# Kernel optimization log

Hardware: AMD Instinct MI355X
Metric: run time of the kernel (lower is better)

The kernel has to match this reference:

```python
import jax, jax.numpy as jnp
import numpy as np

EPS = 1e-5

def _mlp(x, W1, b1, W2, b2):
    h = jax.nn.gelu(x @ W1 + b1, approximate=False)
    return h @ W2 + b2

def _ln(x, g, b):
    m = jnp.mean(x, axis=-1, keepdims=True)
    v = jnp.mean((x - m) ** 2, axis=-1, keepdims=True)
    return (x - m) * jax.lax.rsqrt(v + EPS) * g + b

def setup_inputs() -> dict:
    key = jax.random.key(0)
    B, N, D = 4, 256, 128
    ks = jax.random.split(key, 32)
    s = 0.02
    inp = {
        "node_h": jax.random.normal(ks[0], (B, N, D), jnp.float32),
        "pair_h": jax.random.normal(ks[1], (B, N, N, D), jnp.float32),
        "node_mask": jax.random.randint(ks[2], (B, N), 0, 2, jnp.int32),
        "edge_mask": jax.random.randint(ks[3], (B, N, N), 0, 2, jnp.int32),
        # node_from_pair MLP: 3D -> 2D -> D
        "nfp_W1": jax.random.normal(ks[4], (3 * D, 2 * D), jnp.float32) * s,
        "nfp_b1": jnp.zeros((2 * D,), jnp.float32),
        "nfp_W2": jax.random.normal(ks[5], (2 * D, D), jnp.float32) * s,
        "nfp_b2": jnp.zeros((D,), jnp.float32),
        # pair_from_node MLP: 5D -> 2D -> D
        "pfn_W1": jax.random.normal(ks[6], (5 * D, 2 * D), jnp.float32) * s,
        "pfn_b1": jnp.zeros((2 * D,), jnp.float32),
        "pfn_W2": jax.random.normal(ks[7], (2 * D, D), jnp.float32) * s,
        "pfn_b2": jnp.zeros((D,), jnp.float32),
        # node_ff: D -> 4D -> D
        "nff_W1": jax.random.normal(ks[8], (D, 4 * D), jnp.float32) * s,
        "nff_b1": jnp.zeros((4 * D,), jnp.float32),
        "nff_W2": jax.random.normal(ks[9], (4 * D, D), jnp.float32) * s,
        "nff_b2": jnp.zeros((D,), jnp.float32),
        # pair_ff: D -> 4D -> D
        "pff_W1": jax.random.normal(ks[10], (D, 4 * D), jnp.float32) * s,
        "pff_b1": jnp.zeros((4 * D,), jnp.float32),
        "pff_W2": jax.random.normal(ks[11], (4 * D, D), jnp.float32) * s,
        "pff_b2": jnp.zeros((D,), jnp.float32),
        # gates: 2D -> D, sigmoid
        "og_W": jax.random.normal(ks[12], (2 * D, D), jnp.float32) * s,
        "og_b": jnp.zeros((D,), jnp.float32),
        "ig_W": jax.random.normal(ks[13], (2 * D, D), jnp.float32) * s,
        "ig_b": jnp.zeros((D,), jnp.float32),
        # LayerNorms
        "nn1_g": jnp.ones((D,), jnp.float32), "nn1_b": jnp.zeros((D,), jnp.float32),
        "nn2_g": jnp.ones((D,), jnp.float32), "nn2_b": jnp.zeros((D,), jnp.float32),
        "pn1_g": jnp.ones((D,), jnp.float32), "pn1_b": jnp.zeros((D,), jnp.float32),
        "pn2_g": jnp.ones((D,), jnp.float32), "pn2_b": jnp.zeros((D,), jnp.float32),
    }
    return inp

def reference(node_h, pair_h, node_mask, edge_mask,
              nfp_W1, nfp_b1, nfp_W2, nfp_b2,
              pfn_W1, pfn_b1, pfn_W2, pfn_b2,
              nff_W1, nff_b1, nff_W2, nff_b2,
              pff_W1, pff_b1, pff_W2, pff_b2,
              og_W, og_b, ig_W, ig_b,
              nn1_g, nn1_b, nn2_g, nn2_b,
              pn1_g, pn1_b, pn2_g, pn2_b):
    vp = edge_mask.astype(jnp.float32)                       # [B,N,N]
    pair_m = pair_h * vp[..., None]                          # masked pairs
    out_deg = jnp.clip(vp.sum(axis=2), 1.0)[..., None]       # [B,N,1]
    in_deg = jnp.clip(vp.sum(axis=1), 1.0)[..., None]        # [B,N,1]
    out_ctx_raw = pair_m.sum(axis=2) / out_deg               # [B,N,D]
    in_ctx_raw = pair_m.sum(axis=1) / in_deg                 # [B,N,D]
    out_g = jax.nn.sigmoid(jnp.concatenate([node_h, out_ctx_raw], -1) @ og_W + og_b)
    in_g = jax.nn.sigmoid(jnp.concatenate([node_h, in_ctx_raw], -1) @ ig_W + ig_b)
    node_upd = _mlp(jnp.concatenate([node_h, out_g * out_ctx_raw, in_g * in_ctx_raw], -1),
                    nfp_W1, nfp_b1, nfp_W2, nfp_b2)
    node_h = _ln(node_h + node_upd, nn1_g, nn1_b)
    node_h = _ln(node_h + _mlp(node_h, nff_W1, nff_b1, nff_W2, nff_b2), nn2_g, nn2_b)
    node_h = node_h * node_mask.astype(jnp.float32)[..., None]

    B, N, D = node_h.shape
    hi = jnp.broadcast_to(node_h[:, :, None, :], (B, N, N, D))
    hj = jnp.broadcast_to(node_h[:, None, :, :], (B, N, N, D))
    feat = jnp.concatenate([pair_h, hi, hj, hi - hj, hi * hj], -1)  # [B,N,N,5D]
    pair_upd = _mlp(feat, pfn_W1, pfn_b1, pfn_W2, pfn_b2)
    pair_h = _ln(pair_h + pair_upd, pn1_g, pn1_b)
    pair_h = _ln(pair_h + _mlp(pair_h, pff_W1, pff_b1, pff_W2, pff_b2), pn2_g, pn2_b)
    pair_h = pair_h * vp[..., None]
    return (node_h, pair_h)
```

## Files before the change

kernel.cpp:

```cpp
#include <hip/hip_runtime.h>
#include <hip/hip_bf16.h>

#define DI __device__ __forceinline__

typedef float f32x4 __attribute__((ext_vector_type(4)));
typedef float f32x2 __attribute__((ext_vector_type(2)));
typedef short s16x8 __attribute__((ext_vector_type(8)));
typedef short s16x4 __attribute__((ext_vector_type(4)));

DI short f2bf(float x) {
  union { float f; unsigned u; } v; v.f = x;
  unsigned r = v.u + 0x7fffu + ((v.u >> 16) & 1u);
  return (short)(r >> 16);
}

DI float bf2f(short x) {
  union { unsigned u; float f; } v;
  v.u = ((unsigned)(unsigned short)x) << 16;
  return v.f;
}

DI float gelu_f(float x) {
  return 0.5f * x * (1.0f + erff(x * 0.70710678118654752f));
}

DI f32x4 mfma16(s16x8 a, s16x8 b, f32x4 c) {
  return __builtin_amdgcn_mfma_f32_16x16x32_bf16(a, b, c, 0, 0, 0);
}

__global__ __launch_bounds__(256) void prep_kernel(
    const float* __restrict__ pfnW1, const float* __restrict__ pfnW2,
    const float* __restrict__ pffW1, const float* __restrict__ pffW2,
    short* __restrict__ W1b, float* __restrict__ Wu, short* __restrict__ W2T,
    short* __restrict__ W1Tp, short* __restrict__ W2Tp) {
  int idx = blockIdx.x * 256 + threadIdx.x;
  if (idx < 98304) {
    int n = idx / 384, k = idx % 384;
    float v;
    if (k < 128) v = pfnW1[k * 256 + n];
    else if (k < 256) v = pfnW1[(128 + k) * 256 + n] - pfnW1[(256 + k) * 256 + n];
    else v = pfnW1[(256 + k) * 256 + n];
    W1b[idx] = f2bf(v);
    return;
  }
  idx -= 98304;
  if (idx < 32768) {
    int k = idx / 256, n = idx % 256;
    Wu[idx] = pfnW1[(128 + k) * 256 + n] + pfnW1[(384 + k) * 256 + n];
    return;
  }
  idx -= 32768;
  if (idx < 32768) {
    int n = idx / 256, k = idx % 256;
    W2T[idx] = f2bf(pfnW2[k * 128 + n]);
    return;
  }
  idx -= 32768;
  if (idx < 65536) {
    int n = idx / 128, k = idx % 128;
    W1Tp[idx] = f2bf(pffW1[k * 512 + n]);
    return;
  }
  idx -= 65536;
  if (idx < 65536) {
    int n = idx / 512, k = idx % 512;
    W2Tp[idx] = f2bf(pffW2[k * 128 + n]);
  }
}

__global__ __launch_bounds__(256) void ctx_kernel(
    const float* __restrict__ pair_h, const int* __restrict__ edge_mask,
    float* __restrict__ out_ctx, float* __restrict__ in_ctx) {
  __shared__ float sacc[2][128];
  __shared__ float sdeg[2];
  const int wg = blockIdx.x;
  const int t = threadIdx.x;
  const int half = t >> 7, d = t & 127;
  const bool outmode = wg < 1024;
  const int w2 = outmode ? wg : wg - 1024;
  const int b = w2 >> 8, x = w2 & 255;

  float acc = 0.f, deg = 0.f;
  for (int y0 = 0; y0 < 256; y0 += 2) {
    const int y = y0 + half;
    int row;
    if (outmode) row = (b * 256 + x) * 256 + y;
    else row = (b * 256 + y) * 256 + x;
    const int m = edge_mask[row];
    if (m) {
      acc += pair_h[(long)row * 128 + d];
      deg += 1.f;
    }
  }
  sacc[half][d] = acc;
  if (d == 0) sdeg[half] = deg;
  __syncthreads();
  if (t < 128) {
    float tot = sacc[0][d] + sacc[1][d];
    float dg = fmaxf(sdeg[0] + sdeg[1], 1.f);
    float* dst = outmode ? out_ctx : in_ctx;
    dst[(b * 256 + x) * 128 + d] = tot / dg;
  }
}

__global__ __launch_bounds__(256) void node_kernel(
    const float* __restrict__ node_h, const float* __restrict__ out_ctx,
    const float* __restrict__ in_ctx, const int* __restrict__ node_mask,
    const float* __restrict__ ogW, const float* __restrict__ ogb,
    const float* __restrict__ igW, const float* __restrict__ igb,
    const float* __restrict__ nW1, const float* __restrict__ nb1,
    const float* __restrict__ nW2, const float* __restrict__ nb2,
    const float* __restrict__ fW1, const float* __restrict__ fb1,
    const float* __restrict__ fW2, const float* __restrict__ fb2,
    const float* __restrict__ g1, const float* __restrict__ be1,
    const float* __restrict__ g2, const float* __restrict__ be2,
    float* __restrict__ out_node, short* __restrict__ node_bf) {
  __shared__ float sh[4][1792];
  const int t = threadIdx.x;
  const int wv = t >> 6, lane = t & 63;
  float* const xn = sh[wv];
  float* const xo = sh[wv] + 256;
  float* const xi = sh[wv] + 512;
  float* const hh = sh[wv] + 768;
  const int row0 = blockIdx.x * 8 + wv * 2;

#pragma unroll
  for (int r = 0; r < 2; ++r) {
    const int row = row0 + r;
#pragma unroll
    for (int c = 0; c < 2; ++c) {
      const int col = lane + 64 * c;
      xn[r * 128 + col] = node_h[row * 128 + col];
      xo[r * 128 + col] = out_ctx[row * 128 + col];
      xi[r * 128 + col] = in_ctx[row * 128 + col];
    }
  }
  __syncthreads();

  {
    float ao[2][2], ai[2][2];
#pragma unroll
    for (int c = 0; c < 2; ++c) {
      const int col = lane + 64 * c;
      ao[0][c] = ao[1][c] = ogb[col];
      ai[0][c] = ai[1][c] = igb[col];
    }
    for (int k = 0; k < 256; ++k) {
      float xo0, xo1, xi0, xi1;
      if (k < 128) {
        xo0 = xi0 = xn[k];
        xo1 = xi1 = xn[128 + k];
      } else {
        xo0 = xo[k - 128]; xo1 = xo[k];
        xi0 = xi[k - 128]; xi1 = xi[k];
      }
#pragma unroll
      for (int c = 0; c < 2; ++c) {
        const int col = lane + 64 * c;
        const float wo = ogW[k * 128 + col], wi = igW[k * 128 + col];
        ao[0][c] += xo0 * wo; ao[1][c] += xo1 * wo;
        ai[0][c] += xi0 * wi; ai[1][c] += xi1 * wi;
      }
    }
#pragma unroll
    for (int c = 0; c < 2; ++c) {
      const int col = lane + 64 * c;
#pragma unroll
      for (int r = 0; r < 2; ++r) {
        const float go = 1.f / (1.f + __expf(-ao[r][c]));
        const float gi = 1.f / (1.f + __expf(-ai[r][c]));
        xo[r * 128 + col] *= go;
        xi[r * 128 + col] *= gi;
      }
    }
  }
  __syncthreads();

  {
    float a1[2][4];
#pragma unroll
    for (int c = 0; c < 4; ++c) {
      const int col = lane + 64 * c;
      a1[0][c] = a1[1][c] = nb1[col];
    }
    for (int k = 0; k < 384; ++k) {
      const float* src = (k < 128) ? xn : (k < 256) ? xo : xi;
      const int kk = k & 127;
      const float x0 = src[kk], x1 = src[128 + kk];
#pragma unroll
      for (int c = 0; c < 4; ++c) {
        const int col = lane + 64 * c;
        const float w = nW1[k * 256 + col];
        a1[0][c] += x0 * w; a1[1][c] += x1 * w;
      }
    }
#pragma unroll
    for (int c = 0; c < 4; ++c) {
      const int col = lane + 64 * c;
      hh[col] = gelu_f(a1[0][c]);
      hh[512 + col] = gelu_f(a1[1][c]);
    }
  }
  __syncthreads();
  {
    float a2[2][2];
#pragma unroll
    for (int c = 0; c < 2; ++c) {
      const int col = lane + 64 * c;
      a2[0][c] = a2[1][c] = nb2[col];
    }
    for (int k = 0; k < 256; ++k) {
      const float h0 = hh[k], h1 = hh[512 + k];
#pragma unroll
      for (int c = 0; c < 2; ++c) {
        const int col = lane + 64 * c;
        const float w = nW2[k * 128 + col];
        a2[0][c] += h0 * w; a2[1][c] += h1 * w;
      }
    }
#pragma unroll
    for (int r = 0; r < 2; ++r) {
      float v0 = xn[r * 128 + lane] + a2[r][0];
      float v1 = xn[r * 128 + lane + 64] + a2[r][1];
      float s = v0 + v1, ss = v0 * v0 + v1 * v1;
#pragma unroll
      for (int off = 1; off < 64; off <<= 1) {
        s += __shfl_xor(s, off, 64);
        ss += __shfl_xor(ss, off, 64);
      }
      const float m = s * (1.f / 128.f);
      const float var = ss * (1.f / 128.f) - m * m;
      const float rs = rsqrtf(var + 1e-5f);
      xn[r * 128 + lane] = (v0 - m) * rs * g1[lane] + be1[lane];
      xn[r * 128 + lane + 64] = (v1 - m) * rs * g1[lane + 64] + be1[lane + 64];
    }
  }
  __syncthreads();

  {
    float af[2][8];
#pragma unroll
    for (int c = 0; c < 8; ++c) {
      const int col = lane + 64 * c;
      af[0][c] = af[1][c] = fb1[col];
    }
    for (int k = 0; k < 128; ++k) {
      const float x0 = xn[k], x1 = xn[128 + k];
#pragma unroll
      for (int c = 0; c < 8; ++c) {
        const int col = lane + 64 * c;
        const float w = fW1[k * 512 + col];
        af[0][c] += x0 * w; af[1][c] += x1 * w;
      }
    }
#pragma unroll
    for (int c = 0; c < 8; ++c) {
      const int col = lane + 64 * c;
      hh[col] = gelu_f(af[0][c]);
      hh[512 + col] = gelu_f(af[1][c]);
    }
  }
  __syncthreads();
  {
    float a2[2][2];
#pragma unroll
    for (int c = 0; c < 2; ++c) {
      const int col = lane + 64 * c;
      a2[0][c] = a2[1][c] = fb2[col];
    }
    for (int k = 0; k < 512; ++k) {
      const float h0 = hh[k], h1 = hh[512 + k];
#pragma unroll
      for (int c = 0; c < 2; ++c) {
        const int col = lane + 64 * c;
        const float w = fW2[k * 128 + col];
        a2[0][c] += h0 * w; a2[1][c] += h1 * w;
      }
    }
#pragma unroll
    for (int r = 0; r < 2; ++r) {
      const int row = row0 + r;
      float v0 = xn[r * 128 + lane] + a2[r][0];
      float v1 = xn[r * 128 + lane + 64] + a2[r][1];
      float s = v0 + v1, ss = v0 * v0 + v1 * v1;
#pragma unroll
      for (int off = 1; off < 64; off <<= 1) {
        s += __shfl_xor(s, off, 64);
        ss += __shfl_xor(ss, off, 64);
      }
      const float m = s * (1.f / 128.f);
      const float var = ss * (1.f / 128.f) - m * m;
      const float rs = rsqrtf(var + 1e-5f);
      const float msk = (float)node_mask[row];
      const float o0 = ((v0 - m) * rs * g2[lane] + be2[lane]) * msk;
      const float o1 = ((v1 - m) * rs * g2[lane + 64] + be2[lane + 64]) * msk;
      out_node[row * 128 + lane] = o0;
      out_node[row * 128 + lane + 64] = o1;
      node_bf[row * 128 + lane] = f2bf(o0);
      node_bf[row * 128 + lane + 64] = f2bf(o1);
    }
  }
}

__global__ __launch_bounds__(256) void u_kernel(
    const float* __restrict__ out_node, const float* __restrict__ Wu,
    const float* __restrict__ b1, float* __restrict__ u_all) {
  __shared__ float nrow[8][128];
  const int t = threadIdx.x;
  const int r0 = blockIdx.x * 8;
  {
    const int r = t >> 5, c = (t & 31) * 4;
    *(f32x4*)&nrow[r][c] = *(const f32x4*)(out_node + (r0 + r) * 128 + c);
  }
  __syncthreads();
  float acc[8];
  const float bb = b1[t];
#pragma unroll
  for (int r = 0; r < 8; ++r) acc[r] = bb;
  for (int k = 0; k < 128; ++k) {
    const float w = Wu[k * 256 + t];
#pragma unroll
    for (int r = 0; r < 8; ++r) acc[r] += nrow[r][k] * w;
  }
#pragma unroll
  for (int r = 0; r < 8; ++r) u_all[(r0 + r) * 256 + t] = acc[r];
}

__global__ __launch_bounds__(512, 4) void pair_kernel(
    const float* __restrict__ pair_h, const short* __restrict__ node_bf,
    const int* __restrict__ edge_mask, const short* __restrict__ W1b,
    const short* __restrict__ W2T, const short* __restrict__ W1Tp,
    const short* __restrict__ W2Tp, const float* __restrict__ u_all,
    const float* __restrict__ b2, const float* __restrict__ b1p,
    const float* __restrict__ b2p, const float* __restrict__ g1,
    const float* __restrict__ be1, const float* __restrict__ g2,
    const float* __restrict__ be2, float* __restrict__ out_pair) {
  constexpr int OFF_A = 0, OFF_H1 = 0, OFF_Y = 0, OFF_H2 = 16384,
                OFF_SCR = 49152;
  __shared__ __align__(16) char smem[81920];

  const int t = threadIdx.x;
  const int wg = blockIdx.x;
  const int b = wg >> 10, rem = wg & 1023;
  const int i = rem >> 2, j0 = (rem & 3) << 6;
  const int bi = (b << 8) + i;
  const long rowbase = (long)bi * 256 + j0;

  const int lane = t & 63, wv = t >> 6;
  const int lr = lane & 15, lq = lane >> 4;
  const int swz = (lr & 7) << 4;

  {
    const int r = t >> 3, oc = t & 7, c0 = oc * 16;
    const int rsw = (r & 7) << 4;
    const float* prow = pair_h + (rowbase + r) * 128 + c0;
    const short* hjrow = node_bf + (b * 256 + j0 + r) * 128 + c0;
    const short* hirow = node_bf + (b * 256 + i) * 128 + c0;
    char* arow = smem + OFF_A + r * 768;
    s16x8 pr[2], hj[2], hi[2];
#pragma unroll
    for (int h = 0; h < 2; ++h) {
      f32x4 p0 = *(const f32x4*)(prow + h * 8);
      f32x4 p1 = *(const f32x4*)(prow + h * 8 + 4);
      s16x8 sp;
#pragma unroll
      for (int e = 0; e < 4; ++e) { sp[e] = f2bf(p0[e]); sp[e + 4] = f2bf(p1[e]); }
      pr[h] = sp;
      hj[h] = *(const s16x8*)(hjrow + h * 8);
      hi[h] = *(const s16x8*)(hirow + h * 8);
    }
#pragma unroll
    for (int h = 0; h < 2; ++h) {
      *(s16x8*)(arow + ((c0 * 2 + h * 16) ^ rsw)) = pr[h];
      *(s16x8*)(arow + ((256 + c0 * 2 + h * 16) ^ rsw)) = hj[h];
      s16x8 pd;
#pragma unroll
      for (int e = 0; e < 8; ++e) pd[e] = f2bf(bf2f(hi[h][e]) * bf2f(hj[h][e]));
      *(s16x8*)(arow + ((512 + c0 * 2 + h * 16) ^ rsw)) = pd;
    }
  }
  __syncthreads();

  f32x4 acc1[4][2];
#pragma unroll
  for (int jt = 0; jt < 4; ++jt)
#pragma unroll
    for (int nt = 0; nt < 2; ++nt) acc1[jt][nt] = {0.f, 0.f, 0.f, 0.f};
  {
    const int nb = wv * 32;
    const short* wp0 = W1b + (nb + lr) * 384 + lq * 8;
    const short* wp1 = W1b + (nb + 16 + lr) * 384 + lq * 8;
    s16x8 w0 = *(const s16x8*)wp0;
    s16x8 w1 = *(const s16x8*)wp1;
#pragma unroll
    for (int ks = 0; ks < 12; ++ks) {
      s16x8 nw0 = w0, nw1 = w1;
      if (ks < 11) {
        nw0 = *(const s16x8*)(wp0 + (ks + 1) * 32);
        nw1 = *(const s16x8*)(wp1 + (ks + 1) * 32);
      }
      s16x8 d[4];
#pragma unroll
      for (int jt = 0; jt < 4; ++jt)
        d[jt] = *(const s16x8*)(smem + OFF_A +
                                (((jt * 16 + lr) * 768 + ks * 64 + lq * 16) ^ swz));
#pragma unroll
      for (int jt = 0; jt < 4; ++jt) {
        acc1[jt][0] = mfma16(w0, d[jt], acc1[jt][0]);
        acc1[jt][1] = mfma16(w1, d[jt], acc1[jt][1]);
      }
      w0 = nw0; w1 = nw1;
    }
  }
  __syncthreads();
  {
    const int nb = wv * 32;
#pragma unroll
    for (int nt = 0; nt < 2; ++nt) {
      const int n0 = nb + nt * 16 + lq * 4;
      f32x4 bu = *(const f32x4*)(u_all + bi * 256 + n0);
#pragma unroll
      for (int jt = 0; jt < 4; ++jt) {
        const int j = jt * 16 + lr;
        s16x4 hp;
#pragma unroll
        for (int v = 0; v < 4; ++v) hp[v] = f2bf(gelu_f(acc1[jt][nt][v] + bu[v]));
        *(s16x4*)(smem + OFF_H1 + ((j * 512 + n0 * 2) ^ swz)) = hp;
      }
    }
  }
  __syncthreads();

  const int jb = (wv >> 2) * 32, nb2 = (wv & 3) * 32;
  f32x4 x1v[2][2];
  {
    f32x4 acc2[2][2];
#pragma unroll
    for (int jt = 0; jt < 2; ++jt)
#pragma unroll
      for (int nt = 0; nt < 2; ++nt) acc2[jt][nt] = {0.f, 0.f, 0.f, 0.f};
    const short* wp0 = W2T + (nb2 + lr) * 256 + lq * 8;
    const short* wp1 = W2T + (nb2 + 16 + lr) * 256 + lq * 8;
    s16x8 w0 = *(const s16x8*)wp0;
    s16x8 w1 = *(const s16x8*)wp1;
#pragma unroll
    for (int ks = 0; ks < 8; ++ks) {
      s16x8 nw0 = w0, nw1 = w1;
      if (ks < 7) {
        nw0 = *(const s16x8*)(wp0 + (ks + 1) * 32);
        nw1 = *(const s16x8*)(wp1 + (ks + 1) * 32);
      }
      s16x8 d[2];
#pragma unroll
      for (int jt = 0; jt < 2; ++jt)
        d[jt] = *(const s16x8*)(smem + OFF_H1 +
                                (((jb + jt * 16 + lr) * 512 + ks * 64 + lq * 16) ^ swz));
#pragma unroll
      for (int jt = 0; jt < 2; ++jt) {
        acc2[jt][0] = mfma16(w0, d[jt], acc2[jt][0]);
        acc2[jt][1] = mfma16(w1, d[jt], acc2[jt][1]);
      }
      w0 = nw0; w1 = nw1;
    }
#pragma unroll
    for (int nt = 0; nt < 2; ++nt) {
      const int n0 = nb2 + nt * 16 + lq * 4;
      f32x4 bv = *(const f32x4*)(b2 + n0);
#pragma unroll
      for (int jt = 0; jt < 2; ++jt) {
        const int j = jb + jt * 16 + lr;
        f32x4 pr = *(const f32x4*)(pair_h + (rowbase + j) * 128 + n0);
        x1v[jt][nt] = acc2[jt][nt] + bv + pr;
      }
    }
  }
  {
    float s[2], ss[2];
#pragma unroll
    for (int jt = 0; jt < 2; ++jt) {
      s[jt] = 0.f; ss[jt] = 0.f;
#pragma unroll
      for (int nt = 0; nt < 2; ++nt)
#pragma unroll
        for (int v = 0; v < 4; ++v) {
          const float x = x1v[jt][nt][v];
          s[jt] += x; ss[jt] += x * x;
        }
      s[jt] += __shfl_xor(s[jt], 16, 64);
      ss[jt] += __shfl_xor(ss[jt], 16, 64);
      s[jt] += __shfl_xor(s[jt], 32, 64);
      ss[jt] += __shfl_xor(ss[jt], 32, 64);
    }
    if (lq == 0) {
#pragma unroll
      for (int jt = 0; jt < 2; ++jt) {
        const int j = jb + jt * 16 + lr;
        f32x2 p = {s[jt], ss[jt]};
        *(f32x2*)(smem + OFF_SCR + j * 32 + (wv & 3) * 8) = p;
      }
    }
    __syncthreads();
    float lnm[2], lnr[2];
#pragma unroll
    for (int jt = 0; jt < 2; ++jt) {
      const int j = jb + jt * 16 + lr;
      f32x4 pA = *(const f32x4*)(smem + OFF_SCR + j * 32);
      f32x4 pB = *(const f32x4*)(smem + OFF_SCR + j * 32 + 16);
      const float S = pA[0] + pA[2] + pB[0] + pB[2];
      const float SS = pA[1] + pA[3] + pB[1] + pB[3];
      const float m = S * (1.f / 128.f);
      const float var = SS * (1.f / 128.f) - m * m;
      lnm[jt] = m;
      lnr[jt] = rsqrtf(var + 1e-5f);
    }
#pragma unroll
    for (int nt = 0; nt < 2; ++nt) {
      const int n0 = nb2 + nt * 16 + lq * 4;
      f32x4 gv = *(const f32x4*)(g1 + n0);
      f32x4 bv = *(const f32x4*)(be1 + n0);
#pragma unroll
      for (int jt = 0; jt < 2; ++jt) {
        const int j = jb + jt * 16 + lr;
        s16x4 yp;
#pragma unroll
        for (int v = 0; v < 4; ++v)
          yp[v] = f2bf((x1v[jt][nt][v] - lnm[jt]) * lnr[jt] * gv[v] + bv[v]);
        *(s16x4*)(smem + OFF_Y + ((j * 256 + n0 * 2) ^ swz)) = yp;
      }
    }
  }
  __syncthreads();

#pragma unroll
  for (int p = 0; p < 2; ++p) {
    f32x4 acc3[4][2];
#pragma unroll
    for (int jt = 0; jt < 4; ++jt)
#pragma unroll
      for (int nt = 0; nt < 2; ++nt) acc3[jt][nt] = {0.f, 0.f, 0.f, 0.f};
    const int nb3 = wv * 64 + p * 32;
    const short* wp0 = W1Tp + (nb3 + lr) * 128 + lq * 8;
    const short* wp1 = W1Tp + (nb3 + 16 + lr) * 128 + lq * 8;
    s16x8 w0 = *(const s16x8*)wp0;
    s16x8 w1 = *(const s16x8*)wp1;
#pragma unroll
    for (int ks = 0; ks < 4; ++ks) {
      s16x8 nw0 = w0, nw1 = w1;
      if (ks < 3) {
        nw0 = *(const s16x8*)(wp0 + (ks + 1) * 32);
        nw1 = *(const s16x8*)(wp1 + (ks + 1) * 32);
      }
      s16x8 d[4];
#pragma unroll
      for (int jt = 0; jt < 4; ++jt)
        d[jt] = *(const s16x8*)(smem + OFF_Y +
                                (((jt * 16 + lr) * 256 + ks * 64 + lq * 16) ^ swz));
#pragma unroll
      for (int jt = 0; jt < 4; ++jt) {
        acc3[jt][0] = mfma16(w0, d[jt], acc3[jt][0]);
        acc3[jt][1] = mfma16(w1, d[jt], acc3[jt][1]);
      }
      w0 = nw0; w1 = nw1;
    }
#pragma unroll
    for (int nt = 0; nt < 2; ++nt) {
      const int n0 = nb3 + nt * 16 + lq * 4;
      f32x4 bv = *(const f32x4*)(b1p + n0);
#pragma unroll
      for (int jt = 0; jt < 4; ++jt) {
        const int j = jt * 16 + lr;
        s16x4 hp;
#pragma unroll
        for (int v = 0; v < 4; ++v) hp[v] = f2bf(gelu_f(acc3[jt][nt][v] + bv[v]));
        *(s16x4*)(smem + OFF_H2 + ((j * 1024 + n0 * 2) ^ swz)) = hp;
      }
    }
  }
  __syncthreads();

  f32x4 x2v[2][2];
  {
    f32x4 acc4[2][2];
#pragma unroll
    for (int jt = 0; jt < 2; ++jt)
#pragma unroll
      for (int nt = 0; nt < 2; ++nt) acc4[jt][nt] = {0.f, 0.f, 0.f, 0.f};
    const short* wp0 = W2Tp + (nb2 + lr) * 512 + lq * 8;
    const short* wp1 = W2Tp + (nb2 + 16 + lr) * 512 + lq * 8;
    s16x8 w0 = *(const s16x8*)wp0;
    s16x8 w1 = *(const s16x8*)wp1;
#pragma unroll
    for (int ks = 0; ks < 16; ++ks) {
      s16x8 nw0 = w0, nw1 = w1;
      if (ks < 15) {
        nw0 = *(const s16x8*)(wp0 + (ks + 1) * 32);
        nw1 = *(const s16x8*)(wp1 + (ks + 1) * 32);
      }
      s16x8 d[2];
#pragma unroll
      for (int jt = 0; jt < 2; ++jt)
        d[jt] = *(const s16x8*)(smem + OFF_H2 +
                                (((jb + jt * 16 + lr) * 1024 + ks * 64 + lq * 16) ^ swz));
#pragma unroll
      for (int jt = 0; jt < 2; ++jt) {
        acc4[jt][0] = mfma16(w0, d[jt], acc4[jt][0]);
        acc4[jt][1] = mfma16(w1, d[jt], acc4[jt][1]);
      }
      w0 = nw0; w1 = nw1;
    }
#pragma unroll
    for (int nt = 0; nt < 2; ++nt) {
      const int n0 = nb2 + nt * 16 + lq * 4;
      f32x4 bv = *(const f32x4*)(b2p + n0);
#pragma unroll
      for (int jt = 0; jt < 2; ++jt) {
        const int j = jb + jt * 16 + lr;
        s16x4 yv = *(const s16x4*)(smem + OFF_Y + ((j * 256 + n0 * 2) ^ swz));
        f32x4 yr;
#pragma unroll
        for (int v = 0; v < 4; ++v) yr[v] = bf2f(yv[v]);
        x2v[jt][nt] = acc4[jt][nt] + bv + yr;
      }
    }
  }
  {
    float s[2], ss[2];
#pragma unroll
    for (int jt = 0; jt < 2; ++jt) {
      s[jt] = 0.f; ss[jt] = 0.f;
#pragma unroll
      for (int nt = 0; nt < 2; ++nt)
#pragma unroll
        for (int v = 0; v < 4; ++v) {
          const float x = x2v[jt][nt][v];
          s[jt] += x; ss[jt] += x * x;
        }
      s[jt] += __shfl_xor(s[jt], 16, 64);
      ss[jt] += __shfl_xor(ss[jt], 16, 64);
      s[jt] += __shfl_xor(s[jt], 32, 64);
      ss[jt] += __shfl_xor(ss[jt], 32, 64);
    }
    __syncthreads();
    if (lq == 0) {
#pragma unroll
      for (int jt = 0; jt < 2; ++jt) {
        const int j = jb + jt * 16 + lr;
        f32x2 p = {s[jt], ss[jt]};
        *(f32x2*)(smem + OFF_SCR + j * 32 + (wv & 3) * 8) = p;
      }
    }
    __syncthreads();
    float lnm[2], lnr[2], vp[2];
#pragma unroll
    for (int jt = 0; jt < 2; ++jt) {
      const int j = jb + jt * 16 + lr;
      f32x4 pA = *(const f32x4*)(smem + OFF_SCR + j * 32);
      f32x4 pB = *(const f32x4*)(smem + OFF_SCR + j * 32 + 16);
      const float S = pA[0] + pA[2] + pB[0] + pB[2];
      const float SS = pA[1] + pA[3] + pB[1] + pB[3];
      const float m = S * (1.f / 128.f);
      const float var = SS * (1.f / 128.f) - m * m;
      lnm[jt] = m;
      lnr[jt] = rsqrtf(var + 1e-5f);
      vp[jt] = (float)edge_mask[(long)bi * 256 + j0 + j];
    }
#pragma unroll
    for (int nt = 0; nt < 2; ++nt) {
      const int n0 = nb2 + nt * 16 + lq * 4;
      f32x4 gv = *(const f32x4*)(g2 + n0);
      f32x4 bv = *(const f32x4*)(be2 + n0);
#pragma unroll
      for (int jt = 0; jt < 2; ++jt) {
        const int j = jb + jt * 16 + lr;
        f32x4 o;
#pragma unroll
        for (int v = 0; v < 4; ++v)
          o[v] = ((x2v[jt][nt][v] - lnm[jt]) * lnr[jt] * gv[v] + bv[v]) * vp[jt];
        *(f32x4*)(out_pair + (rowbase + j) * 128 + n0) = o;
      }
    }
  }
}

extern "C" void kernel_launch(void* const* d_in, const int* in_sizes, int n_in,
                              void* d_out, int out_size, void* d_ws,
                              size_t ws_size, hipStream_t stream) {
  const float* node_h = (const float*)d_in[0];
  const float* pair_h = (const float*)d_in[1];
  const int* node_mask = (const int*)d_in[2];
  const int* edge_mask = (const int*)d_in[3];
  const float* nfp_W1 = (const float*)d_in[4];
  const float* nfp_b1 = (const float*)d_in[5];
  const float* nfp_W2 = (const float*)d_in[6];
  const float* nfp_b2 = (const float*)d_in[7];
  const float* pfn_W1 = (const float*)d_in[8];
  const float* pfn_b1 = (const float*)d_in[9];
  const float* pfn_W2 = (const float*)d_in[10];
  const float* pfn_b2 = (const float*)d_in[11];
  const float* nff_W1 = (const float*)d_in[12];
  const float* nff_b1 = (const float*)d_in[13];
  const float* nff_W2 = (const float*)d_in[14];
  const float* nff_b2 = (const float*)d_in[15];
  const float* pff_W1 = (const float*)d_in[16];
  const float* pff_b1 = (const float*)d_in[17];
  const float* pff_W2 = (const float*)d_in[18];
  const float* pff_b2 = (const float*)d_in[19];
  const float* og_W = (const float*)d_in[20];
  const float* og_b = (const float*)d_in[21];
  const float* ig_W = (const float*)d_in[22];
  const float* ig_b = (const float*)d_in[23];
  const float* nn1_g = (const float*)d_in[24];
  const float* nn1_b = (const float*)d_in[25];
  const float* nn2_g = (const float*)d_in[26];
  const float* nn2_b = (const float*)d_in[27];
  const float* pn1_g = (const float*)d_in[28];
  const float* pn1_b = (const float*)d_in[29];
  const float* pn2_g = (const float*)d_in[30];
  const float* pn2_b = (const float*)d_in[31];

  char* ws = (char*)d_ws;
  short* W1b = (short*)(ws);
  short* W2T = (short*)(ws + 196608);
  short* W1Tp = (short*)(ws + 262144);
  short* W2Tp = (short*)(ws + 393216);
  float* Wu = (float*)(ws + 524288);
  float* out_ctx = (float*)(ws + 655360);
  float* in_ctx = (float*)(ws + 1179648);
  short* node_bf = (short*)(ws + 1703936);
  float* u_all = (float*)(ws + 1966080);

  float* out_node = (float*)d_out;
  float* out_pair = (float*)d_out + 131072;

  prep_kernel<<<1152, 256, 0, stream>>>(pfn_W1, pfn_W2, pff_W1, pff_W2, W1b,
                                        Wu, W2T, W1Tp, W2Tp);
  ctx_kernel<<<2048, 256, 0, stream>>>(pair_h, edge_mask, out_ctx, in_ctx);
  node_kernel<<<128, 256, 0, stream>>>(
      node_h, out_ctx, in_ctx, node_mask, og_W, og_b, ig_W, ig_b, nfp_W1,
      nfp_b1, nfp_W2, nfp_b2, nff_W1, nff_b1, nff_W2, nff_b2, nn1_g, nn1_b,
      nn2_g, nn2_b, out_node, node_bf);
  u_kernel<<<128, 256, 0, stream>>>(out_node, Wu, pfn_b1, u_all);
  pair_kernel<<<4096, 512, 0, stream>>>(
      pair_h, node_bf, edge_mask, W1b, W2T, W1Tp, W2Tp, u_all, pfn_b2, pff_b1,
      pff_b2, pn1_g, pn1_b, pn2_g, pn2_b, out_pair);
}
```

Before: 625.4 us.

## Split pair FF into two K-halves, shrink LDS, fuse small kernels, fast GELU

```diff
diff --git a/kernel.cpp b/kernel.cpp
--- a/kernel.cpp
+++ b/kernel.cpp
@@ -7,6 +7,8 @@
 typedef float f32x2 __attribute__((ext_vector_type(2)));
 typedef short s16x8 __attribute__((ext_vector_type(8)));
 typedef short s16x4 __attribute__((ext_vector_type(4)));
+typedef unsigned u32x2 __attribute__((ext_vector_type(2)));
+typedef unsigned u32x4 __attribute__((ext_vector_type(4)));
 
 DI short f2bf(float x) {
   union { float f; unsigned u; } v; v.f = x;
@@ -20,66 +22,75 @@
   return v.f;
 }
 
+DI unsigned cvt_pk(float lo, float hi) {
+  unsigned r;
+  asm("v_cvt_pk_bf16_f32 %0, %1, %2" : "=v"(r) : "v"(lo), "v"(hi));
+  return r;
+}
+
+DI s16x8 pack8(f32x4 a, f32x4 b) {
+  union { u32x4 u; s16x8 s; } r;
+  r.u[0] = cvt_pk(a[0], a[1]); r.u[1] = cvt_pk(a[2], a[3]);
+  r.u[2] = cvt_pk(b[0], b[1]); r.u[3] = cvt_pk(b[2], b[3]);
+  return r.s;
+}
+
 DI float gelu_f(float x) {
-  return 0.5f * x * (1.0f + erff(x * 0.70710678118654752f));
-}
-
-DI f32x4 mfma16(s16x8 a, s16x8 b, f32x4 c) {
-  return __builtin_amdgcn_mfma_f32_16x16x32_bf16(a, b, c, 0, 0, 0);
-}
-
-__global__ __launch_bounds__(256) void prep_kernel(
+  const float e = __expf(-x * fmaf(x * x, 0.0713548162f, 1.5957691216f));
+  return __fdividef(x, 1.f + e);
+}
+
+__global__ __launch_bounds__(256) void prep_ctx_kernel(
+    const float* __restrict__ pair_h, const int* __restrict__ edge_mask,
     const float* __restrict__ pfnW1, const float* __restrict__ pfnW2,
     const float* __restrict__ pffW1, const float* __restrict__ pffW2,
     short* __restrict__ W1b, float* __restrict__ Wu, short* __restrict__ W2T,
-    short* __restrict__ W1Tp, short* __restrict__ W2Tp) {
-  int idx = blockIdx.x * 256 + threadIdx.x;
-  if (idx < 98304) {
-    int n = idx / 384, k = idx % 384;
-    float v;
-    if (k < 128) v = pfnW1[k * 256 + n];
-    else if (k < 256) v = pfnW1[(128 + k) * 256 + n] - pfnW1[(256 + k) * 256 + n];
-    else v = pfnW1[(256 + k) * 256 + n];
-    W1b[idx] = f2bf(v);
-    return;
-  }
-  idx -= 98304;
-  if (idx < 32768) {
-    int k = idx / 256, n = idx % 256;
-    Wu[idx] = pfnW1[(128 + k) * 256 + n] + pfnW1[(384 + k) * 256 + n];
-    return;
-  }
-  idx -= 32768;
-  if (idx < 32768) {
-    int n = idx / 256, k = idx % 256;
-    W2T[idx] = f2bf(pfnW2[k * 128 + n]);
-    return;
-  }
-  idx -= 32768;
-  if (idx < 65536) {
-    int n = idx / 128, k = idx % 128;
-    W1Tp[idx] = f2bf(pffW1[k * 512 + n]);
-    return;
-  }
-  idx -= 65536;
-  if (idx < 65536) {
-    int n = idx / 512, k = idx % 512;
-    W2Tp[idx] = f2bf(pffW2[k * 128 + n]);
-  }
-}
-
-__global__ __launch_bounds__(256) void ctx_kernel(
-    const float* __restrict__ pair_h, const int* __restrict__ edge_mask,
+    short* __restrict__ W1Tp, short* __restrict__ W2Tp,
     float* __restrict__ out_ctx, float* __restrict__ in_ctx) {
   __shared__ float sacc[2][128];
   __shared__ float sdeg[2];
+  const int t = threadIdx.x;
+  if (blockIdx.x >= 2048) {
+    int idx = (blockIdx.x - 2048) * 256 + t;
+    if (idx < 98304) {
+      int n = idx / 384, k = idx % 384;
+      float v;
+      if (k < 128) v = pfnW1[k * 256 + n];
+      else if (k < 256) v = pfnW1[(128 + k) * 256 + n] - pfnW1[(256 + k) * 256 + n];
+      else v = pfnW1[(256 + k) * 256 + n];
+      W1b[idx] = f2bf(v);
+      return;
+    }
+    idx -= 98304;
+    if (idx < 32768) {
+      int k = idx / 256, n = idx % 256;
+      Wu[idx] = pfnW1[(128 + k) * 256 + n] + pfnW1[(384 + k) * 256 + n];
+      return;
+    }
+    idx -= 32768;
+    if (idx < 32768) {
+      int n = idx / 256, k = idx % 256;
+      W2T[idx] = f2bf(pfnW2[k * 128 + n]);
+      return;
+    }
+    idx -= 32768;
+    if (idx < 65536) {
+      int n = idx / 128, k = idx % 128;
+      W1Tp[idx] = f2bf(pffW1[k * 512 + n]);
+      return;
+    }
+    idx -= 65536;
+    if (idx < 65536) {
+      int n = idx / 512, k = idx % 512;
+      W2Tp[idx] = f2bf(pffW2[k * 128 + n]);
+    }
+    return;
+  }
   const int wg = blockIdx.x;
-  const int t = threadIdx.x;
   const int half = t >> 7, d = t & 127;
   const bool outmode = wg < 1024;
   const int w2 = outmode ? wg : wg - 1024;
   const int b = w2 >> 8, x = w2 & 255;
-
   float acc = 0.f, deg = 0.f;
   for (int y0 = 0; y0 < 256; y0 += 2) {
     const int y = y0 + half;
@@ -114,8 +125,11 @@
     const float* __restrict__ fW2, const float* __restrict__ fb2,
     const float* __restrict__ g1, const float* __restrict__ be1,
     const float* __restrict__ g2, const float* __restrict__ be2,
-    float* __restrict__ out_node, short* __restrict__ node_bf) {
+    const float* __restrict__ Wu, const float* __restrict__ ub1,
+    float* __restrict__ out_node, short* __restrict__ node_bf,
+    float* __restrict__ u_all) {
   __shared__ float sh[4][1792];
+  __shared__ float fin[8][128];
   const int t = threadIdx.x;
   const int wv = t >> 6, lane = t & 63;
   float* const xn = sh[wv];
@@ -298,35 +312,29 @@
       out_node[row * 128 + lane + 64] = o1;
       node_bf[row * 128 + lane] = f2bf(o0);
       node_bf[row * 128 + lane + 64] = f2bf(o1);
-    }
-  }
-}
-
-__global__ __launch_bounds__(256) void u_kernel(
-    const float* __restrict__ out_node, const float* __restrict__ Wu,
-    const float* __restrict__ b1, float* __restrict__ u_all) {
-  __shared__ float nrow[8][128];
-  const int t = threadIdx.x;
-  const int r0 = blockIdx.x * 8;
-  {
-    const int r = t >> 5, c = (t & 31) * 4;
-    *(f32x4*)&nrow[r][c] = *(const f32x4*)(out_node + (r0 + r) * 128 + c);
-  }
-  __syncthreads();
-  float acc[8];
-  const float bb = b1[t];
-#pragma unroll
-  for (int r = 0; r < 8; ++r) acc[r] = bb;
-  for (int k = 0; k < 128; ++k) {
-    const float w = Wu[k * 256 + t];
-#pragma unroll
-    for (int r = 0; r < 8; ++r) acc[r] += nrow[r][k] * w;
-  }
-#pragma unroll
-  for (int r = 0; r < 8; ++r) u_all[(r0 + r) * 256 + t] = acc[r];
-}
-
-__global__ __launch_bounds__(512, 4) void pair_kernel(
+      fin[wv * 2 + r][lane] = o0;
+      fin[wv * 2 + r][lane + 64] = o1;
+    }
+  }
+  __syncthreads();
+  {
+    float uacc[8];
+    const float bb = ub1[t];
+#pragma unroll
+    for (int r = 0; r < 8; ++r) uacc[r] = bb;
+#pragma unroll 4
+    for (int k = 0; k < 128; ++k) {
+      const float w = Wu[k * 256 + t];
+#pragma unroll
+      for (int r = 0; r < 8; ++r) uacc[r] += fin[r][k] * w;
+    }
+#pragma unroll
+    for (int r = 0; r < 8; ++r)
+      u_all[(blockIdx.x * 8 + r) * 256 + t] = uacc[r];
+  }
+}
+
+__global__ __launch_bounds__(512, 6) void pair_kernel(
     const float* __restrict__ pair_h, const short* __restrict__ node_bf,
     const int* __restrict__ edge_mask, const short* __restrict__ W1b,
     const short* __restrict__ W2T, const short* __restrict__ W1Tp,
@@ -337,7 +345,7 @@
     const float* __restrict__ be2, float* __restrict__ out_pair) {
   constexpr int OFF_A = 0, OFF_H1 = 0, OFF_Y = 0, OFF_H2 = 16384,
                 OFF_SCR = 49152;
-  __shared__ __align__(16) char smem[81920];
+  __shared__ __align__(16) char smem[51200];
 
   const int t = threadIdx.x;
   const int wg = blockIdx.x;
@@ -357,26 +365,20 @@
     const short* hjrow = node_bf + (b * 256 + j0 + r) * 128 + c0;
     const short* hirow = node_bf + (b * 256 + i) * 128 + c0;
     char* arow = smem + OFF_A + r * 768;
-    s16x8 pr[2], hj[2], hi[2];
 #pragma unroll
     for (int h = 0; h < 2; ++h) {
       f32x4 p0 = *(const f32x4*)(prow + h * 8);
       f32x4 p1 = *(const f32x4*)(prow + h * 8 + 4);
-      s16x8 sp;
-#pragma unroll
-      for (int e = 0; e < 4; ++e) { sp[e] = f2bf(p0[e]); sp[e + 4] = f2bf(p1[e]); }
-      pr[h] = sp;
-      hj[h] = *(const s16x8*)(hjrow + h * 8);
-      hi[h] = *(const s16x8*)(hirow + h * 8);
-    }
-#pragma unroll
-    for (int h = 0; h < 2; ++h) {
-      *(s16x8*)(arow + ((c0 * 2 + h * 16) ^ rsw)) = pr[h];
-      *(s16x8*)(arow + ((256 + c0 * 2 + h * 16) ^ rsw)) = hj[h];
-      s16x8 pd;
-#pragma unroll
-      for (int e = 0; e < 8; ++e) pd[e] = f2bf(bf2f(hi[h][e]) * bf2f(hj[h][e]));
-      *(s16x8*)(arow + ((512 + c0 * 2 + h * 16) ^ rsw)) = pd;
+      s16x8 hj = *(const s16x8*)(hjrow + h * 8);
+      s16x8 hi = *(const s16x8*)(hirow + h * 8);
+      *(s16x8*)(arow + ((c0 * 2 + h * 16) ^ rsw)) = pack8(p0, p1);
+      *(s16x8*)(arow + ((256 + c0 * 2 + h * 16) ^ rsw)) = hj;
+      union { u32x4 u; s16x8 s; } pd;
+#pragma unroll
+      for (int e = 0; e < 4; ++e)
+        pd.u[e] = cvt_pk(bf2f(hi[2 * e]) * bf2f(hj[2 * e]),
+                         bf2f(hi[2 * e + 1]) * bf2f(hj[2 * e + 1]));
+      *(s16x8*)(arow + ((512 + c0 * 2 + h * 16) ^ rsw)) = pd.s;
     }
   }
   __syncthreads();
@@ -406,8 +408,8 @@
                                 (((jt * 16 + lr) * 768 + ks * 64 + lq * 16) ^ swz));
 #pragma unroll
       for (int jt = 0; jt < 4; ++jt) {
-        acc1[jt][0] = mfma16(w0, d[jt], acc1[jt][0]);
-        acc1[jt][1] = mfma16(w1, d[jt], acc1[jt][1]);
+        acc1[jt][0] = __builtin_amdgcn_mfma_f32_16x16x32_bf16(w0, d[jt], acc1[jt][0], 0, 0, 0);
+        acc1[jt][1] = __builtin_amdgcn_mfma_f32_16x16x32_bf16(w1, d[jt], acc1[jt][1], 0, 0, 0);
       }
       w0 = nw0; w1 = nw1;
     }
@@ -422,10 +424,11 @@
 #pragma unroll
       for (int jt = 0; jt < 4; ++jt) {
         const int j = jt * 16 + lr;
-        s16x4 hp;
-#pragma unroll
-        for (int v = 0; v < 4; ++v) hp[v] = f2bf(gelu_f(acc1[jt][nt][v] + bu[v]));
-        *(s16x4*)(smem + OFF_H1 + ((j * 512 + n0 * 2) ^ swz)) = hp;
+        u32x2 pk = {cvt_pk(gelu_f(acc1[jt][nt][0] + bu[0]),
+                           gelu_f(acc1[jt][nt][1] + bu[1])),
+                    cvt_pk(gelu_f(acc1[jt][nt][2] + bu[2]),
+                           gelu_f(acc1[jt][nt][3] + bu[3]))};
+        *(u32x2*)(smem + OFF_H1 + ((j * 512 + n0 * 2) ^ swz)) = pk;
       }
     }
   }
@@ -457,8 +460,8 @@
                                 (((jb + jt * 16 + lr) * 512 + ks * 64 + lq * 16) ^ swz));
 #pragma unroll
       for (int jt = 0; jt < 2; ++jt) {
-        acc2[jt][0] = mfma16(w0, d[jt], acc2[jt][0]);
-        acc2[jt][1] = mfma16(w1, d[jt], acc2[jt][1]);
+        acc2[jt][0] = __builtin_amdgcn_mfma_f32_16x16x32_bf16(w0, d[jt], acc2[jt][0], 0, 0, 0);
+        acc2[jt][1] = __builtin_amdgcn_mfma_f32_16x16x32_bf16(w1, d[jt], acc2[jt][1], 0, 0, 0);
       }
       w0 = nw0; w1 = nw1;
     }
@@ -521,15 +524,22 @@
 #pragma unroll
       for (int jt = 0; jt < 2; ++jt) {
         const int j = jb + jt * 16 + lr;
-        s16x4 yp;
+        float y[4];
 #pragma unroll
         for (int v = 0; v < 4; ++v)
-          yp[v] = f2bf((x1v[jt][nt][v] - lnm[jt]) * lnr[jt] * gv[v] + bv[v]);
-        *(s16x4*)(smem + OFF_Y + ((j * 256 + n0 * 2) ^ swz)) = yp;
-      }
-    }
-  }
-  __syncthreads();
+          y[v] = (x1v[jt][nt][v] - lnm[jt]) * lnr[jt] * gv[v] + bv[v];
+        u32x2 pk = {cvt_pk(y[0], y[1]), cvt_pk(y[2], y[3])};
+        *(u32x2*)(smem + OFF_Y + ((j * 256 + n0 * 2) ^ swz)) = pk;
+      }
+    }
+  }
+  __syncthreads();
+
+  f32x4 acc4[2][2];
+#pragma unroll
+  for (int jt = 0; jt < 2; ++jt)
+#pragma unroll
+    for (int nt = 0; nt < 2; ++nt) acc4[jt][nt] = {0.f, 0.f, 0.f, 0.f};
 
 #pragma unroll
   for (int p = 0; p < 2; ++p) {
@@ -538,89 +548,78 @@
     for (int jt = 0; jt < 4; ++jt)
 #pragma unroll
       for (int nt = 0; nt < 2; ++nt) acc3[jt][nt] = {0.f, 0.f, 0.f, 0.f};
-    const int nb3 = wv * 64 + p * 32;
-    const short* wp0 = W1Tp + (nb3 + lr) * 128 + lq * 8;
-    const short* wp1 = W1Tp + (nb3 + 16 + lr) * 128 + lq * 8;
-    s16x8 w0 = *(const s16x8*)wp0;
-    s16x8 w1 = *(const s16x8*)wp1;
-#pragma unroll
-    for (int ks = 0; ks < 4; ++ks) {
-      s16x8 nw0 = w0, nw1 = w1;
-      if (ks < 3) {
-        nw0 = *(const s16x8*)(wp0 + (ks + 1) * 32);
-        nw1 = *(const s16x8*)(wp1 + (ks + 1) * 32);
-      }
-      s16x8 d[4];
-#pragma unroll
-      for (int jt = 0; jt < 4; ++jt)
-        d[jt] = *(const s16x8*)(smem + OFF_Y +
-                                (((jt * 16 + lr) * 256 + ks * 64 + lq * 16) ^ swz));
-#pragma unroll
-      for (int jt = 0; jt < 4; ++jt) {
-        acc3[jt][0] = mfma16(w0, d[jt], acc3[jt][0]);
-        acc3[jt][1] = mfma16(w1, d[jt], acc3[jt][1]);
-      }
-      w0 = nw0; w1 = nw1;
-    }
-#pragma unroll
-    for (int nt = 0; nt < 2; ++nt) {
-      const int n0 = nb3 + nt * 16 + lq * 4;
-      f32x4 bv = *(const f32x4*)(b1p + n0);
-#pragma unroll
-      for (int jt = 0; jt < 4; ++jt) {
-        const int j = jt * 16 + lr;
-        s16x4 hp;
-#pragma unroll
-        for (int v = 0; v < 4; ++v) hp[v] = f2bf(gelu_f(acc3[jt][nt][v] + bv[v]));
-        *(s16x4*)(smem + OFF_H2 + ((j * 1024 + n0 * 2) ^ swz)) = hp;
-      }
-    }
-  }
-  __syncthreads();
+    {
+      const int nb3 = p * 256 + wv * 32;
+      const short* wp0 = W1Tp + (nb3 + lr) * 128 + lq * 8;
+      const short* wp1 = W1Tp + (nb3 + 16 + lr) * 128 + lq * 8;
+#pragma unroll
+      for (int ks = 0; ks < 4; ++ks) {
+        s16x8 w0 = *(const s16x8*)(wp0 + ks * 32);
+        s16x8 w1 = *(const s16x8*)(wp1 + ks * 32);
+        s16x8 d[4];
+#pragma unroll
+        for (int jt = 0; jt < 4; ++jt)
+          d[jt] = *(const s16x8*)(smem + OFF_Y +
+                                  (((jt * 16 + lr) * 256 + ks * 64 + lq * 16) ^ swz));
+#pragma unroll
+        for (int jt = 0; jt < 4; ++jt) {
+          acc3[jt][0] = __builtin_amdgcn_mfma_f32_16x16x32_bf16(w0, d[jt], acc3[jt][0], 0, 0, 0);
+          acc3[jt][1] = __builtin_amdgcn_mfma_f32_16x16x32_bf16(w1, d[jt], acc3[jt][1], 0, 0, 0);
+        }
+      }
+    }
+    if (p == 1) __syncthreads();
+    {
+#pragma unroll
+      for (int nt = 0; nt < 2; ++nt) {
+        const int n0l = wv * 32 + nt * 16 + lq * 4;
+        f32x4 bv = *(const f32x4*)(b1p + p * 256 + n0l);
+#pragma unroll
+        for (int jt = 0; jt < 4; ++jt) {
+          const int j = jt * 16 + lr;
+          u32x2 pk = {cvt_pk(gelu_f(acc3[jt][0][0] * 0.f + acc3[jt][nt][0] + bv[0]),
+                             gelu_f(acc3[jt][nt][1] + bv[1])),
+                      cvt_pk(gelu_f(acc3[jt][nt][2] + bv[2]),
+                             gelu_f(acc3[jt][nt][3] + bv[3]))};
+          *(u32x2*)(smem + OFF_H2 + ((j * 512 + n0l * 2) ^ swz)) = pk;
+        }
+      }
+    }
+    __syncthreads();
+    {
+      const short* qp0 = W2Tp + (nb2 + lr) * 512 + p * 256 + lq * 8;
+      const short* qp1 = W2Tp + (nb2 + 16 + lr) * 512 + p * 256 + lq * 8;
+#pragma unroll
+      for (int ks = 0; ks < 8; ++ks) {
+        s16x8 w0 = *(const s16x8*)(qp0 + ks * 32);
+        s16x8 w1 = *(const s16x8*)(qp1 + ks * 32);
+        s16x8 d[2];
+#pragma unroll
+        for (int jt = 0; jt < 2; ++jt)
+          d[jt] = *(const s16x8*)(smem + OFF_H2 +
+                                  (((jb + jt * 16 + lr) * 512 + ks * 64 + lq * 16) ^ swz));
+#pragma unroll
+        for (int jt = 0; jt < 2; ++jt) {
+          acc4[jt][0] = __builtin_amdgcn_mfma_f32_16x16x32_bf16(w0, d[jt], acc4[jt][0], 0, 0, 0);
+          acc4[jt][1] = __builtin_amdgcn_mfma_f32_16x16x32_bf16(w1, d[jt], acc4[jt][1], 0, 0, 0);
+        }
+      }
+    }
+  }
 
   f32x4 x2v[2][2];
-  {
-    f32x4 acc4[2][2];
-#pragma unroll
-    for (int jt = 0; jt < 2; ++jt)
-#pragma unroll
-      for (int nt = 0; nt < 2; ++nt) acc4[jt][nt] = {0.f, 0.f, 0.f, 0.f};
-    const short* wp0 = W2Tp + (nb2 + lr) * 512 + lq * 8;
-    const short* wp1 = W2Tp + (nb2 + 16 + lr) * 512 + lq * 8;
-    s16x8 w0 = *(const s16x8*)wp0;
-    s16x8 w1 = *(const s16x8*)wp1;
-#pragma unroll
-    for (int ks = 0; ks < 16; ++ks) {
-      s16x8 nw0 = w0, nw1 = w1;
-      if (ks < 15) {
-        nw0 = *(const s16x8*)(wp0 + (ks + 1) * 32);
-        nw1 = *(const s16x8*)(wp1 + (ks + 1) * 32);
-      }
-      s16x8 d[2];
-#pragma unroll
-      for (int jt = 0; jt < 2; ++jt)
-        d[jt] = *(const s16x8*)(smem + OFF_H2 +
-                                (((jb + jt * 16 + lr) * 1024 + ks * 64 + lq * 16) ^ swz));
-#pragma unroll
-      for (int jt = 0; jt < 2; ++jt) {
-        acc4[jt][0] = mfma16(w0, d[jt], acc4[jt][0]);
-        acc4[jt][1] = mfma16(w1, d[jt], acc4[jt][1]);
-      }
-      w0 = nw0; w1 = nw1;
-    }
-#pragma unroll
-    for (int nt = 0; nt < 2; ++nt) {
-      const int n0 = nb2 + nt * 16 + lq * 4;
-      f32x4 bv = *(const f32x4*)(b2p + n0);
-#pragma unroll
-      for (int jt = 0; jt < 2; ++jt) {
-        const int j = jb + jt * 16 + lr;
-        s16x4 yv = *(const s16x4*)(smem + OFF_Y + ((j * 256 + n0 * 2) ^ swz));
-        f32x4 yr;
-#pragma unroll
-        for (int v = 0; v < 4; ++v) yr[v] = bf2f(yv[v]);
-        x2v[jt][nt] = acc4[jt][nt] + bv + yr;
-      }
+#pragma unroll
+  for (int nt = 0; nt < 2; ++nt) {
+    const int n0 = nb2 + nt * 16 + lq * 4;
+    f32x4 bv = *(const f32x4*)(b2p + n0);
+#pragma unroll
+    for (int jt = 0; jt < 2; ++jt) {
+      const int j = jb + jt * 16 + lr;
+      s16x4 yv = *(const s16x4*)(smem + OFF_Y + ((j * 256 + n0 * 2) ^ swz));
+      f32x4 yr;
+#pragma unroll
+      for (int v = 0; v < 4; ++v) yr[v] = bf2f(yv[v]);
+      x2v[jt][nt] = acc4[jt][nt] + bv + yr;
     }
   }
   {
@@ -732,14 +731,13 @@
   float* out_node = (float*)d_out;
   float* out_pair = (float*)d_out + 131072;
 
-  prep_kernel<<<1152, 256, 0, stream>>>(pfn_W1, pfn_W2, pff_W1, pff_W2, W1b,
-                                        Wu, W2T, W1Tp, W2Tp);
-  ctx_kernel<<<2048, 256, 0, stream>>>(pair_h, edge_mask, out_ctx, in_ctx);
+  prep_ctx_kernel<<<3200, 256, 0, stream>>>(
+      pair_h, edge_mask, pfn_W1, pfn_W2, pff_W1, pff_W2, W1b, Wu, W2T, W1Tp,
+      W2Tp, out_ctx, in_ctx);
   node_kernel<<<128, 256, 0, stream>>>(
       node_h, out_ctx, in_ctx, node_mask, og_W, og_b, ig_W, ig_b, nfp_W1,
       nfp_b1, nfp_W2, nfp_b2, nff_W1, nff_b1, nff_W2, nff_b2, nn1_g, nn1_b,
-      nn2_g, nn2_b, out_node, node_bf);
-  u_kernel<<<128, 256, 0, stream>>>(out_node, Wu, pfn_b1, u_all);
+      nn2_g, nn2_b, Wu, pfn_b1, out_node, node_bf, u_all);
   pair_kernel<<<4096, 512, 0, stream>>>(
       pair_h, node_bf, edge_mask, W1b, W2T, W1Tp, W2Tp, u_all, pfn_b2, pff_b1,
       pff_b2, pn1_g, pn1_b, pn2_g, pn2_b, out_pair);
```

Result: slower. 728.6 us (+16.5%).
